# Kernel tuning notes

Hardware: AMD Instinct MI355X
Metric: run time of the kernel (lower is better)

The kernel has to match this reference:

```python
import jax, jax.numpy as jnp
import numpy as np

B, S, D, DK = 8, 2048, 768, 214
DROPOUT_P = 0.1


def setup_inputs() -> dict:
    key = jax.random.key(0)
    ks = jax.random.split(key, 11)
    x1 = jax.random.normal(ks[0], (B, S, D), jnp.float32)
    x2 = jax.random.normal(ks[1], (B, S, D), jnp.float32)
    x3 = jax.random.normal(ks[2], (B, S, D), jnp.float32)
    Wq = jax.random.normal(ks[3], (DK, D), jnp.float32) * (1.0 / np.sqrt(D))
    bq = jax.random.normal(ks[4], (DK,), jnp.float32) * 0.01
    Wk = jax.random.normal(ks[5], (DK, D), jnp.float32) * (1.0 / np.sqrt(D))
    bk = jax.random.normal(ks[6], (DK,), jnp.float32) * 0.01
    Wv = jax.random.normal(ks[7], (D, D), jnp.float32) * (1.0 / np.sqrt(D))
    bv = jax.random.normal(ks[8], (D,), jnp.float32) * 0.01
    # full-tensor elementwise divisor: uniform(0,1) + 1, as in the source
    inv_scale = jax.random.uniform(ks[9], (S, S), jnp.float32) + 1.0
    # deterministic inverted-dropout mask, keep prob = 1 - p
    keep = 1.0 - DROPOUT_P
    dropout_mask = (jax.random.uniform(ks[10], (B, S, S)) < keep).astype(jnp.float32) / keep
    return dict(x1=x1, x2=x2, x3=x3, Wq=Wq, bq=bq, Wk=Wk, bk=bk,
                Wv=Wv, bv=bv, inv_scale=inv_scale, dropout_mask=dropout_mask)


def reference(x1, x2, x3, Wq, bq, Wk, bk, Wv, bv, inv_scale, dropout_mask):
    q = jnp.einsum('bsd,kd->bsk', x1, Wq) + bq          # [B,S,DK]
    k = jnp.einsum('bsd,kd->bsk', x2, Wk) + bk          # [B,S,DK]
    v = jnp.einsum('bsd,ed->bse', x3, Wv) + bv          # [B,S,D]
    attn = jnp.einsum('bsk,btk->bst', q, k)             # [B,S,S]
    scaled = attn / inv_scale                           # elementwise full-tensor divisor
    p = jax.nn.softmax(scaled, axis=-1) * dropout_mask  # softmax + inverted dropout
    return jnp.einsum('bst,btd->bsd', p, v)             # [B,S,D]
```

## Files before the change

kernel.cpp:

```cpp
#include <hip/hip_runtime.h>
#include <hip/hip_bf16.h>

typedef unsigned short ushort;
typedef unsigned long long u64;
typedef short bf16x8 __attribute__((ext_vector_type(8)));
typedef _Float16 f16x8 __attribute__((ext_vector_type(8)));
typedef float f32x4 __attribute__((ext_vector_type(4)));

#define NB 8
#define SS 2048
#define DD 768
#define DKV 214
#define DKP 224
#define WROWS 256
#define MSHIFT 40.0f

__device__ __forceinline__ float bf2f(ushort u) {
  union { unsigned int i; float f; } v; v.i = ((unsigned int)u) << 16; return v.f;
}
__device__ __forceinline__ ushort f2bf(float f) {
  union { float f; unsigned int i; } v; v.f = f;
  unsigned int x = v.i;
  return (ushort)((x + 0x7fffu + ((x >> 16) & 1u)) >> 16);
}
__device__ __forceinline__ ushort f2h(float f) {
  union { _Float16 h; ushort u; } cv; cv.h = (_Float16)f; return cv.u;
}
__device__ __forceinline__ bf16x8 cvt8v(f32x4 a, f32x4 b) {
  bf16x8 r;
#pragma unroll
  for (int j = 0; j < 4; ++j) { r[j] = (short)f2bf(a[j]); r[j + 4] = (short)f2bf(b[j]); }
  return r;
}
__device__ __forceinline__ f16x8 cvt8h(f32x4 a, f32x4 b) {
  f16x8 r;
#pragma unroll
  for (int j = 0; j < 4; ++j) { r[j] = (_Float16)a[j]; r[j + 4] = (_Float16)b[j]; }
  return r;
}
__device__ __forceinline__ void gload16(const void* g, void* l) {
  __builtin_amdgcn_global_load_lds(
      (const __attribute__((address_space(1))) void*)g,
      (__attribute__((address_space(3))) void*)l, 16, 0, 0);
}

__global__ __launch_bounds__(256)
void prep_sm(const float* __restrict__ dmk, u64* __restrict__ dbits,
             float* __restrict__ Z)
{
  const int tid0 = blockIdx.x * 256 + threadIdx.x;
  const int stride = gridDim.x * 256;
  for (int i = tid0; i < NB * SS; i += stride) Z[i] = 0.f;
  const size_t nwords = (size_t)NB * SS * SS / 64;
  for (size_t wi = tid0; wi < nwords; wi += stride) {
    const f32x4* p = (const f32x4*)(dmk + wi * 64);
    u64 m = 0;
#pragma unroll
    for (int j = 0; j < 16; ++j) {
      f32x4 v = p[j];
#pragma unroll
      for (int q = 0; q < 4; ++q) m |= (v[q] > 0.5f) ? (1ull << (j * 4 + q)) : 0ull;
    }
    dbits[wi] = m;
  }
}

__global__ __launch_bounds__(256)
void prep_w(const float* __restrict__ Wq, const float* __restrict__ Wk,
            const float* __restrict__ Wv,
            ushort* __restrict__ Wqp, ushort* __restrict__ Wkp,
            ushort* __restrict__ Wvb)
{
  const int NW = WROWS * DD;
  const int NV = DD * DD;
  for (int i = blockIdx.x * 256 + threadIdx.x; i < 2 * NW + NV; i += gridDim.x * 256) {
    if (i < NW) {
      int r = i / DD, c = i % DD;
      float v = (r < DKV) ? Wq[i] : 0.f;
      Wqp[(c >> 5) * (WROWS * 32) + r * 32 + (c & 31)] = f2h(v);
    } else if (i < 2 * NW) {
      int j = i - NW;
      int r = j / DD, c = j % DD;
      float v = (r < DKV) ? Wk[j] : 0.f;
      Wkp[(c >> 5) * (WROWS * 32) + r * 32 + (c & 31)] = f2h(v);
    } else {
      int j = i - 2 * NW;
      int r = j / DD, c = j % DD;
      Wvb[(c >> 5) * (DD * 32) + r * 32 + (c & 31)] = f2bf(Wv[j]);
    }
  }
}

__global__ __launch_bounds__(256, 4)
void gemm_qk(const float* __restrict__ x1, const float* __restrict__ x2,
             const ushort* __restrict__ Wqp, const ushort* __restrict__ Wkp,
             const float* __restrict__ bq, const float* __restrict__ bk,
             ushort* __restrict__ Qp, ushort* __restrict__ Kp)
{
  const int m0 = blockIdx.x * 64;
  const int which = blockIdx.y >> 1;
  const int n0 = (blockIdx.y & 1) * 128;
  const int tid = threadIdx.x;
  const int w  = tid >> 6;
  const int l  = tid & 63;
  const int lr = l & 15;
  const int lh = l >> 4;

  const float*  A    = which ? x2 : x1;
  const ushort* Bw   = which ? Wkp : Wqp;
  const float*  bias = which ? bk : bq;
  ushort* Cp = which ? Kp : Qp;

  __shared__ __align__(16) char lds[2][128][64];

  const int srow = (w << 4) + (l >> 2);
  const size_t gc = (size_t)srow * 64 + (size_t)((((l & 3) ^ ((srow >> 1) & 3))) << 4);
  const char* gb = (const char*)Bw + (size_t)n0 * 64;

  const f32x4 fzero = {0.f, 0.f, 0.f, 0.f};
  f32x4 acc[8];
#pragma unroll
  for (int nt = 0; nt < 8; ++nt) acc[nt] = fzero;

  const float* arow = A + (size_t)(m0 + w * 16 + lr) * DD + lh * 8;

#define QKSTAGE(buf, kk) do {                                             \
    size_t ko = (size_t)(kk) * (WROWS * 64);                              \
    gload16(gb + ko + gc,        &lds[buf][w << 4][0]);                   \
    gload16(gb + ko + gc + 4096, &lds[buf][(w << 4) + 64][0]);            \
  } while (0)

  QKSTAGE(0, 0);
  f32x4 pa = *(const f32x4*)(arow);
  f32x4 pb = *(const f32x4*)(arow + 4);
  __syncthreads();

  for (int kk = 0; kk < 24; ++kk) {
    const int buf = kk & 1;
    if (kk < 23) QKSTAGE(buf ^ 1, kk + 1);
    f32x4 na = fzero, nb = fzero;
    if (kk < 23) {
      na = *(const f32x4*)(arow + (kk + 1) * 32);
      nb = *(const f32x4*)(arow + (kk + 1) * 32 + 4);
    }
    f16x8 af = cvt8h(pa, pb);
#pragma unroll
    for (int nt = 0; nt < 8; ++nt) {
      int br = nt * 16 + lr;
      int bo = (lh ^ ((br >> 1) & 3)) << 4;
      f16x8 wf = *(const f16x8*)&lds[buf][br][bo];
      acc[nt] = __builtin_amdgcn_mfma_f32_16x16x32_f16(af, wf, acc[nt], 0, 0, 0);
    }
    __syncthreads();
    pa = na; pb = nb;
  }
#undef QKSTAGE

#pragma unroll
  for (int nt = 0; nt < 8; ++nt) {
    int n = n0 + nt * 16 + lr;
    if (n >= DKP) continue;
    float bv = (n < DKV) ? bias[n] : 0.f;
#pragma unroll
    for (int r = 0; r < 4; ++r) {
      int m = m0 + w * 16 + lh * 4 + r;
      int bb = m >> 11, s = m & 2047;
      float val = (n < DKV) ? (acc[nt][r] + bv) : 0.f;
      Cp[((size_t)(bb * 7 + (n >> 5)) * SS + s) * 32 + (n & 31)] = f2h(val);
    }
  }
}

__global__ __launch_bounds__(256, 3)
void gemm_v(const float* __restrict__ A, const ushort* __restrict__ Bw,
            const float* __restrict__ bias, ushort* __restrict__ Vp)
{
  const int m0 = blockIdx.x * 64;
  const int n0 = blockIdx.y * 256;
  const int tid = threadIdx.x;
  const int w  = tid >> 6;
  const int l  = tid & 63;
  const int lr = l & 15;
  const int lh = l >> 4;

  __shared__ __align__(16) char smem[36864];
  typedef char VBuf[256][64];
  VBuf* stage = (VBuf*)smem;
  ushort (*lt)[72] = (ushort(*)[72])smem;

  const int srow = (w << 4) + (l >> 2);
  const size_t gc = (size_t)srow * 64 + (size_t)((((l & 3) ^ ((srow >> 1) & 3))) << 4);
  const char* gvw = (const char*)Bw + (size_t)n0 * 64;

  const f32x4 fzero = {0.f, 0.f, 0.f, 0.f};
  f32x4 acc[16];
#pragma unroll
  for (int nt = 0; nt < 16; ++nt) acc[nt] = fzero;

  const float* arow = A + (size_t)(m0 + w * 16 + lr) * DD + lh * 8;

#define VSTAGE(buf, kk) do {                                              \
    size_t ko = (size_t)(kk) * (DD * 64);                                 \
    gload16(gvw + ko + gc,         &stage[buf][w << 4][0]);               \
    gload16(gvw + ko + gc + 4096,  &stage[buf][(w << 4) + 64][0]);        \
    gload16(gvw + ko + gc + 8192,  &stage[buf][(w << 4) + 128][0]);       \
    gload16(gvw + ko + gc + 12288, &stage[buf][(w << 4) + 192][0]);       \
  } while (0)

  VSTAGE(0, 0);
  f32x4 pa = *(const f32x4*)(arow);
  f32x4 pb = *(const f32x4*)(arow + 4);
  __syncthreads();

  for (int kk = 0; kk < 24; ++kk) {
    const int buf = kk & 1;
    if (kk < 23) VSTAGE(buf ^ 1, kk + 1);
    f32x4 na = fzero, nb = fzero;
    if (kk < 23) {
      na = *(const f32x4*)(arow + (kk + 1) * 32);
      nb = *(const f32x4*)(arow + (kk + 1) * 32 + 4);
    }
    bf16x8 af = cvt8v(pa, pb);
#pragma unroll
    for (int nt = 0; nt < 16; ++nt) {
      int br = nt * 16 + lr;
      int bo = (lh ^ ((br >> 1) & 3)) << 4;
      bf16x8 bfr = *(const bf16x8*)&stage[buf][br][bo];
      acc[nt] = __builtin_amdgcn_mfma_f32_16x16x32_bf16(af, bfr, acc[nt], 0, 0, 0);
    }
    __syncthreads();
    pa = na; pb = nb;
  }
#undef VSTAGE

#pragma unroll
  for (int nt = 0; nt < 16; ++nt) {
    int nl = nt * 16 + lr;
    float bv = bias[n0 + nl];
#pragma unroll
    for (int r = 0; r < 4; ++r)
      lt[nl][w * 16 + lh * 4 + r] = f2bf(acc[nt][r] + bv);
  }
  __syncthreads();
  const int bb = m0 >> 11;
  const int s0 = m0 & 2047;
  for (int i = tid; i < 256 * 64; i += 256) {
    int nn = i >> 6, mm = i & 63;
    int d = n0 + nn, t = s0 + mm;
    Vp[((size_t)(bb * 64 + (t >> 5)) * DD + d) * 32 + (t & 31)] = lt[nn][mm];
  }
}

__global__ __launch_bounds__(512, 4)
void gemm_s(const ushort* __restrict__ Qp, const ushort* __restrict__ Kp,
            const float* __restrict__ isc, const u64* __restrict__ dbits,
            ushort* __restrict__ Pp, float* __restrict__ Z)
{
  const int bid = blockIdx.x;
  const int bb = bid & 7;
  const int tt = bid >> 3;
  const int m0 = (tt & 15) * 128;
  const int n0 = (tt >> 4) * 256;
  const int tid = threadIdx.x;
  const int w  = tid >> 6;
  const int l  = tid & 63;
  const int lr = l & 15;
  const int lh = l >> 4;
  const int wm = w & 1;
  const int wn = w >> 1;

  __shared__ __align__(16) char Qb[2][128][64];
  __shared__ __align__(16) char Kb[2][256][64];

  const int srow = (w << 4) + (l >> 2);
  const size_t gc = (size_t)srow * 64 + (size_t)((((l & 3) ^ ((srow >> 1) & 3))) << 4);

  const char* gq = (const char*)Qp + ((size_t)(bb * 7) * SS + m0) * 64;
  const char* gk = (const char*)Kp + ((size_t)(bb * 7) * SS + n0) * 64;

  const f32x4 fzero = {0.f, 0.f, 0.f, 0.f};
  f32x4 acc[4][4];
#pragma unroll
  for (int mf = 0; mf < 4; ++mf)
#pragma unroll
    for (int nf = 0; nf < 4; ++nf) acc[mf][nf] = fzero;

#define SSTAGE(buf, kk) do {                                            \
    size_t ko = (size_t)(kk) * (SS * 64);                               \
    gload16(gq + ko + gc,        &Qb[buf][w << 4][0]);                  \
    gload16(gk + ko + gc,        &Kb[buf][w << 4][0]);                  \
    gload16(gk + ko + gc + 8192, &Kb[buf][(w << 4) + 128][0]);          \
  } while (0)

  SSTAGE(0, 0);
  __syncthreads();
#pragma unroll 1
  for (int t = 0; t < 7; ++t) {
    const int buf = t & 1;
    if (t < 6) SSTAGE(buf ^ 1, t + 1);
    f16x8 bfr[4];
#pragma unroll
    for (int nf = 0; nf < 4; ++nf) {
      int br = wn * 64 + nf * 16 + lr;
      int bo = (lh ^ ((br >> 1) & 3)) << 4;
      bfr[nf] = *(const f16x8*)&Kb[buf][br][bo];
    }
#pragma unroll
    for (int mf = 0; mf < 4; ++mf) {
      int ar = wm * 64 + mf * 16 + lr;
      int ao = (lh ^ ((ar >> 1) & 3)) << 4;
      f16x8 af = *(const f16x8*)&Qb[buf][ar][ao];
#pragma unroll
      for (int nf = 0; nf < 4; ++nf)
        acc[mf][nf] = __builtin_amdgcn_mfma_f32_16x16x32_f16(af, bfr[nf], acc[mf][nf], 0, 0, 0);
    }
    __syncthreads();
  }
#undef SSTAGE

  const float KEEPR = 1.0f / 0.9f;
#pragma unroll
  for (int mf = 0; mf < 4; ++mf) {
#pragma unroll
    for (int r = 0; r < 4; ++r) {
      const int sr = m0 + wm * 64 + mf * 16 + lh * 4 + r;
      const u64 wbits = dbits[((size_t)bb * SS + sr) * (SS / 64) + (n0 >> 6) + wn];
      float z = 0.f;
#pragma unroll
      for (int nf = 0; nf < 4; ++nf) {
        const int tc = n0 + wn * 64 + nf * 16 + lr;
        float iv = isc[(size_t)sr * SS + tc];
        float sval = acc[mf][nf][r] * __builtin_amdgcn_rcpf(iv);
        float e = __expf(sval - MSHIFT);
        z += e;
        float pm = ((wbits >> (nf * 16 + lr)) & 1ull) ? (e * KEEPR) : 0.f;
        Pp[((size_t)(bb * 64 + (tc >> 5)) * SS + sr) * 32 + (tc & 31)] = f2bf(pm);
      }
#pragma unroll
      for (int off = 1; off < 16; off <<= 1) z += __shfl_xor(z, off);
      if (lr == 0) atomicAdd(&Z[bb * SS + sr], z);
    }
  }
}

__global__ __launch_bounds__(256, 4)
void gemm_pv(const ushort* __restrict__ Pp, const ushort* __restrict__ Vp,
             const float* __restrict__ Z, float* __restrict__ out)
{
  const int bid = blockIdx.x;
  const int bb = bid & 7;
  const int tt = bid >> 3;
  const int m0 = (tt & 15) * 128;
  const int n0 = (tt >> 4) * 128;
  const int tid = threadIdx.x;
  const int w  = tid >> 6;
  const int l  = tid & 63;
  const int lr = l & 15;
  const int lh = l >> 4;
  const int wm = w & 1;
  const int wn = w >> 1;

  __shared__ __align__(16) char Plb[2][128][64];
  __shared__ __align__(16) char Vlb[2][128][64];

  const int srow = (w << 4) + (l >> 2);
  const size_t gc = (size_t)srow * 64 + (size_t)((((l & 3) ^ ((srow >> 1) & 3))) << 4);

  const char* gpb = (const char*)Pp + ((size_t)(bb * 64) * SS + m0) * 64;
  const char* gvb = (const char*)Vp + ((size_t)(bb * 64) * DD + n0) * 64;

  const f32x4 fzero = {0.f, 0.f, 0.f, 0.f};
  f32x4 acc[4][4];
#pragma unroll
  for (int mf = 0; mf < 4; ++mf)
#pragma unroll
    for (int nf = 0; nf < 4; ++nf) acc[mf][nf] = fzero;

#define PVSTAGE(t) do {                                                   \
    size_t k0 = (size_t)(t) * 2;                                          \
    gload16(gpb + k0 * (SS * 64) + gc,              &Plb[0][w << 4][0]);  \
    gload16(gpb + k0 * (SS * 64) + gc + 4096,       &Plb[0][(w << 4) + 64][0]); \
    gload16(gpb + (k0 + 1) * (SS * 64) + gc,        &Plb[1][w << 4][0]);  \
    gload16(gpb + (k0 + 1) * (SS * 64) + gc + 4096, &Plb[1][(w << 4) + 64][0]); \
    gload16(gvb + k0 * (DD * 64) + gc,              &Vlb[0][w << 4][0]);  \
    gload16(gvb + k0 * (DD * 64) + gc + 4096,       &Vlb[0][(w << 4) + 64][0]); \
    gload16(gvb + (k0 + 1) * (DD * 64) + gc,        &Vlb[1][w << 4][0]);  \
    gload16(gvb + (k0 + 1) * (DD * 64) + gc + 4096, &Vlb[1][(w << 4) + 64][0]); \
  } while (0)

  PVSTAGE(0);
  __syncthreads();
#pragma unroll 1
  for (int t = 0; t < 32; ++t) {
#pragma unroll
    for (int pk = 0; pk < 2; ++pk) {
      bf16x8 bfr[4];
#pragma unroll
      for (int nf = 0; nf < 4; ++nf) {
        int br = wn * 64 + nf * 16 + lr;
        int bo = (lh ^ ((br >> 1) & 3)) << 4;
        bfr[nf] = *(const bf16x8*)&Vlb[pk][br][bo];
      }
#pragma unroll
      for (int mf = 0; mf < 4; ++mf) {
        int ar = wm * 64 + mf * 16 + lr;
        int ao = (lh ^ ((ar >> 1) & 3)) << 4;
        bf16x8 af = *(const bf16x8*)&Plb[pk][ar][ao];
#pragma unroll
        for (int nf = 0; nf < 4; ++nf)
          acc[mf][nf] = __builtin_amdgcn_mfma_f32_16x16x32_bf16(af, bfr[nf], acc[mf][nf], 0, 0, 0);
      }
    }
    __syncthreads();
    if (t < 31) {
      PVSTAGE(t + 1);
      __syncthreads();
    }
  }
#undef PVSTAGE

#pragma unroll
  for (int mf = 0; mf < 4; ++mf) {
#pragma unroll
    for (int r = 0; r < 4; ++r) {
      const int sr = m0 + wm * 64 + mf * 16 + lh * 4 + r;
      float rz = __builtin_amdgcn_rcpf(Z[bb * SS + sr]);
#pragma unroll
      for (int nf = 0; nf < 4; ++nf) {
        const int dc = n0 + wn * 64 + nf * 16 + lr;
        out[((size_t)bb * SS + sr) * DD + dc] = acc[mf][nf][r] * rz;
      }
    }
  }
}

extern "C" void kernel_launch(void* const* d_in, const int* in_sizes, int n_in,
                              void* d_out, int out_size, void* d_ws, size_t ws_size,
                              hipStream_t stream) {
  const float* x1  = (const float*)d_in[0];
  const float* x2  = (const float*)d_in[1];
  const float* x3  = (const float*)d_in[2];
  const float* Wq  = (const float*)d_in[3];
  const float* bq  = (const float*)d_in[4];
  const float* Wk  = (const float*)d_in[5];
  const float* bk  = (const float*)d_in[6];
  const float* Wv  = (const float*)d_in[7];
  const float* bv  = (const float*)d_in[8];
  const float* isc = (const float*)d_in[9];
  const float* dmk = (const float*)d_in[10];
  float* out = (float*)d_out;

  const size_t QKN = (size_t)NB * 7 * SS * 32;
  const size_t VPN = (size_t)NB * 64 * DD * 32;
  const size_t WN  = (size_t)WROWS * DD;
  const size_t NV  = (size_t)DD * DD;
  const size_t PPN = (size_t)NB * 64 * SS * 32;

  ushort* Qp  = (ushort*)d_ws;
  ushort* Kp  = Qp + QKN;
  ushort* Vp  = Kp + QKN;
  ushort* Wqp = Vp + VPN;
  ushort* Wkp = Wqp + WN;
  ushort* Wvb = Wkp + WN;
  ushort* Pp  = Wvb + NV;
  float*  Zb  = (float*)(Pp + PPN);
  u64*    dbits = (u64*)(Zb + NB * SS);

  dim3 blk(256);
  prep_w<<<dim3(512),  blk, 0, stream>>>(Wq, Wk, Wv, Wqp, Wkp, Wvb);
  prep_sm<<<dim3(2048), blk, 0, stream>>>(dmk, dbits, Zb);
  gemm_qk<<<dim3(256, 4), blk, 0, stream>>>(x1, x2, Wqp, Wkp, bq, bk, Qp, Kp);
  gemm_v <<<dim3(256, 3), blk, 0, stream>>>(x3, Wvb, bv, Vp);
  gemm_s <<<dim3(1024), dim3(512), 0, stream>>>(Qp, Kp, isc, dbits, Pp, Zb);
  gemm_pv<<<dim3(768),  dim3(256), 0, stream>>>(Pp, Vp, Zb, out);
}
```

Measured before the change: 263.1 us.

## Merge prep kernels, retile QK/V GEMM warps to 2x2, reorder PV tile mapping

Fuses the weight-conversion and dropout-bitmask prep kernels into one launch. Reshapes the warp layout in gemm_qk and gemm_v so each warp computes two 16-row M fragments sharing each B fragment, which halves LDS B reads per MFMA. gemm_v moves to 512-thread blocks covering 384 columns, giving 2 column blocks instead of 3. gemm_pv's block-to-tile mapping now runs N-fastest, which changes L2 locality for P tiles. The larger gemm_v tiles raise LDS use and register pressure per block, which may reduce occupancy.

```diff
diff --git a/kernel.cpp b/kernel.cpp
--- a/kernel.cpp
+++ b/kernel.cpp
@@ -45,35 +45,18 @@
 }
 
 __global__ __launch_bounds__(256)
-void prep_sm(const float* __restrict__ dmk, u64* __restrict__ dbits,
-             float* __restrict__ Z)
+void prep_all(const float* __restrict__ dmk, const float* __restrict__ Wq,
+              const float* __restrict__ Wk, const float* __restrict__ Wv,
+              u64* __restrict__ dbits, ushort* __restrict__ Wqp,
+              ushort* __restrict__ Wkp, ushort* __restrict__ Wvb,
+              float* __restrict__ Z)
 {
   const int tid0 = blockIdx.x * 256 + threadIdx.x;
   const int stride = gridDim.x * 256;
   for (int i = tid0; i < NB * SS; i += stride) Z[i] = 0.f;
-  const size_t nwords = (size_t)NB * SS * SS / 64;
-  for (size_t wi = tid0; wi < nwords; wi += stride) {
-    const f32x4* p = (const f32x4*)(dmk + wi * 64);
-    u64 m = 0;
-#pragma unroll
-    for (int j = 0; j < 16; ++j) {
-      f32x4 v = p[j];
-#pragma unroll
-      for (int q = 0; q < 4; ++q) m |= (v[q] > 0.5f) ? (1ull << (j * 4 + q)) : 0ull;
-    }
-    dbits[wi] = m;
-  }
-}
-
-__global__ __launch_bounds__(256)
-void prep_w(const float* __restrict__ Wq, const float* __restrict__ Wk,
-            const float* __restrict__ Wv,
-            ushort* __restrict__ Wqp, ushort* __restrict__ Wkp,
-            ushort* __restrict__ Wvb)
-{
   const int NW = WROWS * DD;
   const int NV = DD * DD;
-  for (int i = blockIdx.x * 256 + threadIdx.x; i < 2 * NW + NV; i += gridDim.x * 256) {
+  for (int i = tid0; i < 2 * NW + NV; i += stride) {
     if (i < NW) {
       int r = i / DD, c = i % DD;
       float v = (r < DKV) ? Wq[i] : 0.f;
@@ -88,6 +71,18 @@
       int r = j / DD, c = j % DD;
       Wvb[(c >> 5) * (DD * 32) + r * 32 + (c & 31)] = f2bf(Wv[j]);
     }
+  }
+  const size_t nwords = (size_t)NB * SS * SS / 64;
+  for (size_t wi = tid0; wi < nwords; wi += stride) {
+    const f32x4* p = (const f32x4*)(dmk + wi * 64);
+    u64 m = 0;
+#pragma unroll
+    for (int j = 0; j < 16; ++j) {
+      f32x4 v = p[j];
+#pragma unroll
+      for (int q = 0; q < 4; ++q) m |= (v[q] > 0.5f) ? (1ull << (j * 4 + q)) : 0ull;
+    }
+    dbits[wi] = m;
   }
 }
 
@@ -105,6 +100,8 @@
   const int l  = tid & 63;
   const int lr = l & 15;
   const int lh = l >> 4;
+  const int wm = w & 1;
+  const int wn = w >> 1;
 
   const float*  A    = which ? x2 : x1;
   const ushort* Bw   = which ? Wkp : Wqp;
@@ -118,11 +115,16 @@
   const char* gb = (const char*)Bw + (size_t)n0 * 64;
 
   const f32x4 fzero = {0.f, 0.f, 0.f, 0.f};
-  f32x4 acc[8];
-#pragma unroll
-  for (int nt = 0; nt < 8; ++nt) acc[nt] = fzero;
-
-  const float* arow = A + (size_t)(m0 + w * 16 + lr) * DD + lh * 8;
+  f32x4 acc[2][4];
+#pragma unroll
+  for (int mf = 0; mf < 2; ++mf)
+#pragma unroll
+    for (int nt = 0; nt < 4; ++nt) acc[mf][nt] = fzero;
+
+  const float* arow[2];
+#pragma unroll
+  for (int mf = 0; mf < 2; ++mf)
+    arow[mf] = A + (size_t)(m0 + wm * 32 + mf * 16 + lr) * DD + lh * 8;
 
 #define QKSTAGE(buf, kk) do {                                             \
     size_t ko = (size_t)(kk) * (WROWS * 64);                              \
@@ -131,120 +133,157 @@
   } while (0)
 
   QKSTAGE(0, 0);
-  f32x4 pa = *(const f32x4*)(arow);
-  f32x4 pb = *(const f32x4*)(arow + 4);
+  f32x4 pa[2], pb[2];
+#pragma unroll
+  for (int mf = 0; mf < 2; ++mf) {
+    pa[mf] = *(const f32x4*)(arow[mf]);
+    pb[mf] = *(const f32x4*)(arow[mf] + 4);
+  }
   __syncthreads();
 
   for (int kk = 0; kk < 24; ++kk) {
     const int buf = kk & 1;
     if (kk < 23) QKSTAGE(buf ^ 1, kk + 1);
-    f32x4 na = fzero, nb = fzero;
+    f32x4 na[2], nb[2];
     if (kk < 23) {
-      na = *(const f32x4*)(arow + (kk + 1) * 32);
-      nb = *(const f32x4*)(arow + (kk + 1) * 32 + 4);
-    }
-    f16x8 af = cvt8h(pa, pb);
-#pragma unroll
-    for (int nt = 0; nt < 8; ++nt) {
-      int br = nt * 16 + lr;
+#pragma unroll
+      for (int mf = 0; mf < 2; ++mf) {
+        na[mf] = *(const f32x4*)(arow[mf] + (kk + 1) * 32);
+        nb[mf] = *(const f32x4*)(arow[mf] + (kk + 1) * 32 + 4);
+      }
+    }
+    f16x8 af[2];
+#pragma unroll
+    for (int mf = 0; mf < 2; ++mf) af[mf] = cvt8h(pa[mf], pb[mf]);
+#pragma unroll
+    for (int nt = 0; nt < 4; ++nt) {
+      int br = wn * 64 + nt * 16 + lr;
       int bo = (lh ^ ((br >> 1) & 3)) << 4;
       f16x8 wf = *(const f16x8*)&lds[buf][br][bo];
-      acc[nt] = __builtin_amdgcn_mfma_f32_16x16x32_f16(af, wf, acc[nt], 0, 0, 0);
+      acc[0][nt] = __builtin_amdgcn_mfma_f32_16x16x32_f16(af[0], wf, acc[0][nt], 0, 0, 0);
+      acc[1][nt] = __builtin_amdgcn_mfma_f32_16x16x32_f16(af[1], wf, acc[1][nt], 0, 0, 0);
     }
     __syncthreads();
-    pa = na; pb = nb;
+    if (kk < 23) {
+#pragma unroll
+      for (int mf = 0; mf < 2; ++mf) { pa[mf] = na[mf]; pb[mf] = nb[mf]; }
+    }
   }
 #undef QKSTAGE
 
 #pragma unroll
-  for (int nt = 0; nt < 8; ++nt) {
-    int n = n0 + nt * 16 + lr;
-    if (n >= DKP) continue;
-    float bv = (n < DKV) ? bias[n] : 0.f;
-#pragma unroll
-    for (int r = 0; r < 4; ++r) {
-      int m = m0 + w * 16 + lh * 4 + r;
-      int bb = m >> 11, s = m & 2047;
-      float val = (n < DKV) ? (acc[nt][r] + bv) : 0.f;
-      Cp[((size_t)(bb * 7 + (n >> 5)) * SS + s) * 32 + (n & 31)] = f2h(val);
-    }
-  }
-}
-
-__global__ __launch_bounds__(256, 3)
+  for (int mf = 0; mf < 2; ++mf) {
+#pragma unroll
+    for (int nt = 0; nt < 4; ++nt) {
+      int n = n0 + wn * 64 + nt * 16 + lr;
+      if (n >= DKP) continue;
+      float bv = (n < DKV) ? bias[n] : 0.f;
+#pragma unroll
+      for (int r = 0; r < 4; ++r) {
+        int m = m0 + wm * 32 + mf * 16 + lh * 4 + r;
+        int bb = m >> 11, s = m & 2047;
+        float val = (n < DKV) ? (acc[mf][nt][r] + bv) : 0.f;
+        Cp[((size_t)(bb * 7 + (n >> 5)) * SS + s) * 32 + (n & 31)] = f2h(val);
+      }
+    }
+  }
+}
+
+__global__ __launch_bounds__(512, 4)
 void gemm_v(const float* __restrict__ A, const ushort* __restrict__ Bw,
             const float* __restrict__ bias, ushort* __restrict__ Vp)
 {
   const int m0 = blockIdx.x * 64;
-  const int n0 = blockIdx.y * 256;
+  const int n0 = blockIdx.y * 384;
   const int tid = threadIdx.x;
   const int w  = tid >> 6;
   const int l  = tid & 63;
   const int lr = l & 15;
   const int lh = l >> 4;
-
-  __shared__ __align__(16) char smem[36864];
-  typedef char VBuf[256][64];
-  VBuf* stage = (VBuf*)smem;
+  const int wm = w & 1;
+  const int wn = w >> 1;
+
+  __shared__ __align__(16) char smem[55296];
   ushort (*lt)[72] = (ushort(*)[72])smem;
 
-  const int srow = (w << 4) + (l >> 2);
-  const size_t gc = (size_t)srow * 64 + (size_t)((((l & 3) ^ ((srow >> 1) & 3))) << 4);
+  const int srow = tid >> 2;
+  const size_t gc = (size_t)srow * 64 + (size_t)((((tid & 3) ^ ((srow >> 1) & 3))) << 4);
   const char* gvw = (const char*)Bw + (size_t)n0 * 64;
 
   const f32x4 fzero = {0.f, 0.f, 0.f, 0.f};
-  f32x4 acc[16];
-#pragma unroll
-  for (int nt = 0; nt < 16; ++nt) acc[nt] = fzero;
-
-  const float* arow = A + (size_t)(m0 + w * 16 + lr) * DD + lh * 8;
+  f32x4 acc[2][6];
+#pragma unroll
+  for (int mf = 0; mf < 2; ++mf)
+#pragma unroll
+    for (int nt = 0; nt < 6; ++nt) acc[mf][nt] = fzero;
+
+  const float* arow[2];
+#pragma unroll
+  for (int mf = 0; mf < 2; ++mf)
+    arow[mf] = A + (size_t)(m0 + wm * 32 + mf * 16 + lr) * DD + lh * 8;
 
 #define VSTAGE(buf, kk) do {                                              \
     size_t ko = (size_t)(kk) * (DD * 64);                                 \
-    gload16(gvw + ko + gc,         &stage[buf][w << 4][0]);               \
-    gload16(gvw + ko + gc + 4096,  &stage[buf][(w << 4) + 64][0]);        \
-    gload16(gvw + ko + gc + 8192,  &stage[buf][(w << 4) + 128][0]);       \
-    gload16(gvw + ko + gc + 12288, &stage[buf][(w << 4) + 192][0]);       \
+    char* db = smem + (buf) * 24576 + (w << 10);                          \
+    gload16(gvw + ko + gc,         db);                                   \
+    gload16(gvw + ko + gc + 8192,  db + 8192);                            \
+    gload16(gvw + ko + gc + 16384, db + 16384);                           \
   } while (0)
 
   VSTAGE(0, 0);
-  f32x4 pa = *(const f32x4*)(arow);
-  f32x4 pb = *(const f32x4*)(arow + 4);
+  f32x4 pa[2], pb[2];
+#pragma unroll
+  for (int mf = 0; mf < 2; ++mf) {
+    pa[mf] = *(const f32x4*)(arow[mf]);
+    pb[mf] = *(const f32x4*)(arow[mf] + 4);
+  }
   __syncthreads();
 
   for (int kk = 0; kk < 24; ++kk) {
     const int buf = kk & 1;
     if (kk < 23) VSTAGE(buf ^ 1, kk + 1);
-    f32x4 na = fzero, nb = fzero;
+    f32x4 na[2], nb[2];
     if (kk < 23) {
-      na = *(const f32x4*)(arow + (kk + 1) * 32);
-      nb = *(const f32x4*)(arow + (kk + 1) * 32 + 4);
-    }
-    bf16x8 af = cvt8v(pa, pb);
-#pragma unroll
-    for (int nt = 0; nt < 16; ++nt) {
-      int br = nt * 16 + lr;
+#pragma unroll
+      for (int mf = 0; mf < 2; ++mf) {
+        na[mf] = *(const f32x4*)(arow[mf] + (kk + 1) * 32);
+        nb[mf] = *(const f32x4*)(arow[mf] + (kk + 1) * 32 + 4);
+      }
+    }
+    bf16x8 af[2];
+#pragma unroll
+    for (int mf = 0; mf < 2; ++mf) af[mf] = cvt8v(pa[mf], pb[mf]);
+#pragma unroll
+    for (int nt = 0; nt < 6; ++nt) {
+      int br = wn * 96 + nt * 16 + lr;
       int bo = (lh ^ ((br >> 1) & 3)) << 4;
-      bf16x8 bfr = *(const bf16x8*)&stage[buf][br][bo];
-      acc[nt] = __builtin_amdgcn_mfma_f32_16x16x32_bf16(af, bfr, acc[nt], 0, 0, 0);
+      bf16x8 bfr = *(const bf16x8*)(smem + buf * 24576 + br * 64 + bo);
+      acc[0][nt] = __builtin_amdgcn_mfma_f32_16x16x32_bf16(af[0], bfr, acc[0][nt], 0, 0, 0);
+      acc[1][nt] = __builtin_amdgcn_mfma_f32_16x16x32_bf16(af[1], bfr, acc[1][nt], 0, 0, 0);
     }
     __syncthreads();
-    pa = na; pb = nb;
+    if (kk < 23) {
+#pragma unroll
+      for (int mf = 0; mf < 2; ++mf) { pa[mf] = na[mf]; pb[mf] = nb[mf]; }
+    }
   }
 #undef VSTAGE
 
 #pragma unroll
-  for (int nt = 0; nt < 16; ++nt) {
-    int nl = nt * 16 + lr;
-    float bv = bias[n0 + nl];
-#pragma unroll
-    for (int r = 0; r < 4; ++r)
-      lt[nl][w * 16 + lh * 4 + r] = f2bf(acc[nt][r] + bv);
+  for (int mf = 0; mf < 2; ++mf) {
+#pragma unroll
+    for (int nt = 0; nt < 6; ++nt) {
+      int nl = wn * 96 + nt * 16 + lr;
+      float bv = bias[n0 + nl];
+#pragma unroll
+      for (int r = 0; r < 4; ++r)
+        lt[nl][wm * 32 + mf * 16 + lh * 4 + r] = f2bf(acc[mf][nt][r] + bv);
+    }
   }
   __syncthreads();
   const int bb = m0 >> 11;
   const int s0 = m0 & 2047;
-  for (int i = tid; i < 256 * 64; i += 256) {
+  for (int i = tid; i < 384 * 64; i += 512) {
     int nn = i >> 6, mm = i & 63;
     int d = n0 + nn, t = s0 + mm;
     Vp[((size_t)(bb * 64 + (t >> 5)) * DD + d) * 32 + (t & 31)] = lt[nn][mm];
@@ -350,8 +389,10 @@
   const int bid = blockIdx.x;
   const int bb = bid & 7;
   const int tt = bid >> 3;
-  const int m0 = (tt & 15) * 128;
-  const int n0 = (tt >> 4) * 128;
+  const int m_idx = tt / 6;
+  const int n_idx = tt - m_idx * 6;
+  const int m0 = m_idx * 128;
+  const int n0 = n_idx * 128;
   const int tid = threadIdx.x;
   const int w  = tid >> 6;
   const int l  = tid & 63;
@@ -467,10 +508,9 @@
   u64*    dbits = (u64*)(Zb + NB * SS);
 
   dim3 blk(256);
-  prep_w<<<dim3(512),  blk, 0, stream>>>(Wq, Wk, Wv, Wqp, Wkp, Wvb);
-  prep_sm<<<dim3(2048), blk, 0, stream>>>(dmk, dbits, Zb);
+  prep_all<<<dim3(2048), blk, 0, stream>>>(dmk, Wq, Wk, Wv, dbits, Wqp, Wkp, Wvb, Zb);
   gemm_qk<<<dim3(256, 4), blk, 0, stream>>>(x1, x2, Wqp, Wkp, bq, bk, Qp, Kp);
-  gemm_v <<<dim3(256, 3), blk, 0, stream>>>(x3, Wvb, bv, Vp);
+  gemm_v <<<dim3(256, 2), dim3(512), 0, stream>>>(x3, Wvb, bv, Vp);
   gemm_s <<<dim3(1024), dim3(512), 0, stream>>>(Qp, Kp, isc, dbits, Pp, Zb);
   gemm_pv<<<dim3(768),  dim3(256), 0, stream>>>(Pp, Vp, Zb, out);
 }
```

Result: slower. 309.0 us (+17.4%).
